# Optimization experiments

Measured on AMD Instinct MI355X. Metric: run time of the kernel, lower is better.

The kernel has to match this reference:

```python
import jax, jax.numpy as jnp
import numpy as np

DIM = 2048
NUM_HEADS = 16
HEAD_DIM = 128
SEQ = 4096
HDIM = NUM_HEADS * HEAD_DIM
EPS = 1e-6


def _rope_tables(seq_len, head_dim):
    quarter = head_dim // 4
    ang = (1.0 / 1024.0) ** np.linspace(0.0, 1.0, quarter, dtype=np.float32)
    ang = np.concatenate([ang, np.zeros(quarter, dtype=np.float32)])  # [head_dim//2]
    theta = np.arange(seq_len, dtype=np.float32)[:, None] * ang[None, :]  # [T, D/2]
    return jnp.asarray(np.cos(theta)), jnp.asarray(np.sin(theta))


def _rms_norm(x):
    return x * jax.lax.rsqrt(jnp.mean(x * x, axis=-1, keepdims=True) + EPS)


def _apply_rope(x, cos, sin):
    # x: [B, T, H, D]; cos/sin: [T, D/2]
    c = cos[None, :, None, :]
    s = sin[None, :, None, :]
    x1, x2 = jnp.split(x, 2, axis=-1)
    return jnp.concatenate([x1 * c + x2 * s, -x1 * s + x2 * c], axis=-1)


def setup_inputs() -> dict:
    key = jax.random.key(0)
    k1, k2, k3, k4, k5 = jax.random.split(key, 5)
    x = jax.random.normal(k1, (1, SEQ, DIM), dtype=jnp.float32)
    ve = jax.random.normal(k2, (1, SEQ, HDIM), dtype=jnp.float32)
    lambdas = jax.random.uniform(k3, (2,), dtype=jnp.float32)
    bound = (3.0 ** 0.5) * 0.5 * DIM ** (-0.5)
    qkv_w = jax.random.uniform(k4, (3, HDIM, DIM), dtype=jnp.float32, minval=-bound, maxval=bound)
    proj_w = 0.02 * jax.random.normal(k5, (DIM, HDIM), dtype=jnp.float32)
    return {"x": x, "ve": ve, "lambdas": lambdas, "qkv_w": qkv_w, "proj_w": proj_w}


def reference(x, ve, lambdas, qkv_w, proj_w):
    B, T, _ = x.shape
    cos, sin = _rope_tables(T, HEAD_DIM)
    # fused QKV projection: qkv_w [3, hdim, dim]
    qkv = jnp.einsum('btd,ced->cbte', x, qkv_w)  # [3, B, T, hdim]
    q, k, v = [a.reshape(B, T, NUM_HEADS, HEAD_DIM) for a in qkv]
    q = _apply_rope(_rms_norm(q), cos, sin)
    k = _apply_rope(_rms_norm(k), cos, sin)
    v = lambdas[0] * v + lambdas[1] * ve.reshape(v.shape)
    # causal SDPA, default scale 1/sqrt(head_dim)
    scale = 1.0 / jnp.sqrt(jnp.float32(HEAD_DIM))
    scores = jnp.einsum('bthd,bshd->bhts', q, k) * scale  # [B, H, T, T]
    causal = jnp.tril(jnp.ones((T, T), dtype=bool))
    scores = jnp.where(causal[None, None], scores, jnp.float32(-1e30))
    probs = jax.nn.softmax(scores, axis=-1)
    out = jnp.einsum('bhts,bshd->bthd', probs, v).reshape(B, T, HDIM)
    return out @ proj_w.T
```

## Files before the change

### kernel.cpp

```cpp
#include <hip/hip_runtime.h>
#include <cstdint>
#include <cstddef>

constexpr int T_SEQ = 4096;
constexpr int NH    = 16;
constexpr int HD    = 128;
constexpr int DIM   = 2048;
constexpr int HDIM  = 2048;

typedef __attribute__((ext_vector_type(8)))  short  short8;
typedef __attribute__((ext_vector_type(4)))  float  f32x4;
typedef __attribute__((ext_vector_type(16))) float  f32x16;
typedef __attribute__((ext_vector_type(8)))  unsigned short u16x8;
typedef __attribute__((ext_vector_type(4)))  unsigned short u16x4;
typedef __attribute__((ext_vector_type(4)))  unsigned uint4v;
typedef __attribute__((ext_vector_type(2)))  int int2v;

__device__ __forceinline__ unsigned short f2bf(float f) {
  unsigned u = __float_as_uint(f);
  return (unsigned short)((u + 0x7FFFu + ((u >> 16) & 1u)) >> 16);
}
__device__ __forceinline__ float bf2f(unsigned short h) {
  return __uint_as_float(((unsigned)h) << 16);
}
__device__ __forceinline__ void gload_lds16(const void* g, void* l) {
  __builtin_amdgcn_global_load_lds((const __attribute__((address_space(1))) void*)g,
                                   (__attribute__((address_space(3))) void*)l, 16, 0, 0);
}
__device__ __forceinline__ int2v plswap(int a, int b) {
  return __builtin_amdgcn_permlane32_swap(a, b, false, false);
}
__device__ __forceinline__ void bar() {
  asm volatile("" ::: "memory");
  __builtin_amdgcn_s_barrier();
  asm volatile("" ::: "memory");
}
#define VMCNT(n) asm volatile("s_waitcnt vmcnt(" #n ")" ::: "memory")

__global__ __launch_bounds__(256) void cvt_f32_bf16(const float* __restrict__ in,
                                                    unsigned short* __restrict__ out, int n4) {
  int i = blockIdx.x * 256 + threadIdx.x;
  if (i < n4) {
    float4 v = ((const float4*)in)[i];
    u16x4 o; o.x = f2bf(v.x); o.y = f2bf(v.y); o.z = f2bf(v.z); o.w = f2bf(v.w);
    ((u16x4*)out)[i] = o;
  }
}

__global__ __launch_bounds__(256) void rope_tables(float* __restrict__ cosT, float* __restrict__ sinT) {
  int idx = blockIdx.x * 256 + threadIdx.x;
  if (idx >= T_SEQ * 64) return;
  int t = idx >> 6, i = idx & 63;
  float ang = (i < 32) ? exp2f(-10.0f * (float)i / 31.0f) : 0.0f;
  float th = (float)t * ang;
  cosT[idx] = cosf(th);
  sinT[idx] = sinf(th);
}

template <int MODE>
__global__ __launch_bounds__(512) void gemm256(const unsigned short* __restrict__ A,
                                               const unsigned short* __restrict__ B,
                                               int K, unsigned short* __restrict__ outb,
                                               float* __restrict__ outf, int N) {
  __shared__ __align__(16) char SM[3 * 49152];
  const int tid = threadIdx.x, w = tid >> 6, lane = tid & 63;
  const int wm = w >> 2, wn = w & 3;
  const int lr = lane >> 4, lc = lane & 15, lc7 = lc & 7;
  const int cpx = gridDim.x >> 3;
  const int idx = (blockIdx.x & 7) * cpx + (blockIdx.x >> 3);
  const int m0 = (idx & 31) * 128, n0 = (idx >> 5) * 256;

  const int arow = lane >> 3;
  const int xcol = ((lane & 7) ^ ((lane >> 3) & 7)) * 8;

  auto stageA = [&](int buf, int t) {
    char* base = SM + buf * 49152;
#pragma unroll
    for (int i = 0; i < 2; i++) {
      int c = w + i * 8;
      gload_lds16(A + (size_t)(m0 + c * 8 + arow) * K + t * 64 + xcol, base + c * 1024);
    }
  };
  auto stageB0 = [&](int buf, int t) {
    char* base = SM + buf * 49152 + 16384;
    gload_lds16(B + (size_t)(n0 + w * 8 + arow) * K + t * 64 + xcol, base + w * 1024);
  };
  auto stageB1 = [&](int buf, int t) {
    char* base = SM + buf * 49152 + 16384;
#pragma unroll
    for (int i = 1; i < 4; i++) {
      int c = w + i * 8;
      gload_lds16(B + (size_t)(n0 + c * 8 + arow) * K + t * 64 + xcol, base + c * 1024);
    }
  };

  f32x4 acc[4][4] = {};
  const int NT = K >> 6;

  stageA(0, 0); stageB0(0, 0); stageB1(0, 0);
  stageA(1, 1); stageB0(1, 1); stageB1(1, 1);
  VMCNT(6);
  bar();

#pragma unroll 1
  for (int t = 0; t < NT; t++) {
    const int c = t % 3, s = (t + 2) % 3;
    const bool st = (t + 2) < NT;
    const char* Ab = SM + c * 49152;
    const char* Bb = Ab + 16384;

    short8 a[4], b[4];
#pragma unroll
    for (int mi = 0; mi < 4; mi++)
      a[mi] = *(const short8*)(Ab + (wm * 64 + mi * 16 + lc) * 128 + ((0 + lr) ^ lc7) * 16);
#pragma unroll
    for (int ni = 0; ni < 4; ni++)
      b[ni] = *(const short8*)(Bb + (wn * 64 + ni * 16 + lc) * 128 + ((0 + lr) ^ lc7) * 16);
    if (st) { stageA(s, t + 2); stageB0(s, t + 2); }
    bar();
    __builtin_amdgcn_s_setprio(1);
#pragma unroll
    for (int mi = 0; mi < 4; mi++)
#pragma unroll
      for (int ni = 0; ni < 4; ni++)
        acc[mi][ni] = __builtin_amdgcn_mfma_f32_16x16x32_bf16(a[mi], b[ni], acc[mi][ni], 0, 0, 0);
    __builtin_amdgcn_s_setprio(0);
    bar();

#pragma unroll
    for (int mi = 0; mi < 4; mi++)
      a[mi] = *(const short8*)(Ab + (wm * 64 + mi * 16 + lc) * 128 + ((4 + lr) ^ lc7) * 16);
#pragma unroll
    for (int ni = 0; ni < 4; ni++)
      b[ni] = *(const short8*)(Bb + (wn * 64 + ni * 16 + lc) * 128 + ((4 + lr) ^ lc7) * 16);
    if (st) stageB1(s, t + 2);
    if (st) { VMCNT(6); } else { VMCNT(0); }
    bar();
    __builtin_amdgcn_s_setprio(1);
#pragma unroll
    for (int mi = 0; mi < 4; mi++)
#pragma unroll
      for (int ni = 0; ni < 4; ni++)
        acc[mi][ni] = __builtin_amdgcn_mfma_f32_16x16x32_bf16(a[mi], b[ni], acc[mi][ni], 0, 0, 0);
    __builtin_amdgcn_s_setprio(0);
    bar();
  }

#pragma unroll
  for (int mi = 0; mi < 4; mi++)
#pragma unroll
    for (int ni = 0; ni < 4; ni++)
#pragma unroll
      for (int r = 0; r < 4; r++) {
        int t = m0 + wm * 64 + mi * 16 + lr * 4 + r;
        int n = n0 + wn * 64 + ni * 16 + lc;
        float v = acc[mi][ni][r];
        if (MODE == 0) {
          int cc = n >> 11, e = n & 2047, h = e >> 7, d = e & 127;
          outb[(((size_t)cc * NH + h) * T_SEQ + t) * HD + d] = f2bf(v);
        } else {
          outf[(size_t)t * N + n] = v;
        }
      }
}

__global__ __launch_bounds__(256) void norm_rope(unsigned short* __restrict__ qkvb,
                                                 const float* __restrict__ cosT,
                                                 const float* __restrict__ sinT) {
  const int tid = threadIdx.x;
  const int li = tid & 15;
  const int row = blockIdx.x * 16 + (tid >> 4);
  const int t = row & (T_SEQ - 1);
  unsigned short* rp = qkvb + (size_t)row * HD + li * 8;
  u16x8 raw = *(const u16x8*)rp;

  float v[8]; float ss = 0.0f;
#pragma unroll
  for (int j = 0; j < 8; j++) { v[j] = bf2f(raw[j]); ss += v[j] * v[j]; }
#pragma unroll
  for (int off = 1; off < 16; off <<= 1) ss += __shfl_xor(ss, off, 16);
  const float rs = rsqrtf(ss * (1.0f / 128.0f) + 1e-6f);

  uint4v rw = __builtin_bit_cast(uint4v, raw);
  uint4v pwv;
  pwv.x = (unsigned)__shfl_xor((int)rw.x, 8, 16);
  pwv.y = (unsigned)__shfl_xor((int)rw.y, 8, 16);
  pwv.z = (unsigned)__shfl_xor((int)rw.z, 8, 16);
  pwv.w = (unsigned)__shfl_xor((int)rw.w, 8, 16);
  u16x8 praw = __builtin_bit_cast(u16x8, pwv);
  float pv[8];
#pragma unroll
  for (int j = 0; j < 8; j++) pv[j] = bf2f(praw[j]);

  const int e0 = (li & 7) * 8;
  const bool hi8 = li >= 8;
  float4 c0 = *(const float4*)(cosT + t * 64 + e0);
  float4 c1 = *(const float4*)(cosT + t * 64 + e0 + 4);
  float4 s0 = *(const float4*)(sinT + t * 64 + e0);
  float4 s1 = *(const float4*)(sinT + t * 64 + e0 + 4);
  float cc[8] = {c0.x, c0.y, c0.z, c0.w, c1.x, c1.y, c1.z, c1.w};
  float sn[8] = {s0.x, s0.y, s0.z, s0.w, s1.x, s1.y, s1.z, s1.w};

  u16x8 o;
#pragma unroll
  for (int j = 0; j < 8; j++) {
    float x1 = hi8 ? pv[j] : v[j];
    float x2 = hi8 ? v[j] : pv[j];
    float r = hi8 ? (-x1 * sn[j] + x2 * cc[j]) : (x1 * cc[j] + x2 * sn[j]);
    o[j] = f2bf(r * rs);
  }
  *(u16x8*)rp = o;
}

__global__ __launch_bounds__(256) void vmix_transpose(const unsigned short* __restrict__ vb,
                                                      const float* __restrict__ ve,
                                                      const float* __restrict__ lam,
                                                      unsigned short* __restrict__ vt) {
  __shared__ float tile[64][65];
  const int h = blockIdx.z, t0 = blockIdx.x * 64, d0 = blockIdx.y * 64;
  const float l0 = lam[0], l1 = lam[1];
  const int tid = threadIdx.x;
  const int tl = tid >> 4, dl4 = (tid & 15) * 4;
#pragma unroll
  for (int i = 0; i < 4; i++) {
    int t_local = tl + i * 16;
    int t = t0 + t_local;
    const unsigned short* vp = vb + ((size_t)h * T_SEQ + t) * HD + d0 + dl4;
    const float* vep = ve + (size_t)t * HDIM + h * HD + d0 + dl4;
    u16x4 vv = *(const u16x4*)vp;
    float4 vef = *(const float4*)vep;
    tile[t_local][dl4 + 0] = l0 * bf2f(vv.x) + l1 * vef.x;
    tile[t_local][dl4 + 1] = l0 * bf2f(vv.y) + l1 * vef.y;
    tile[t_local][dl4 + 2] = l0 * bf2f(vv.z) + l1 * vef.z;
    tile[t_local][dl4 + 3] = l0 * bf2f(vv.w) + l1 * vef.w;
  }
  __syncthreads();
#pragma unroll
  for (int i = 0; i < 2; i++) {
    int idx = tid + i * 256;
    int d_local = idx >> 3, tloc = (idx & 7) * 8;
    u16x8 o;
#pragma unroll
    for (int j = 0; j < 8; j++) o[j] = f2bf(tile[tloc + j][d_local]);
    *(u16x8*)(vt + ((size_t)h * HD + d0 + d_local) * T_SEQ + t0 + tloc) = o;
  }
}

__global__ __launch_bounds__(512)
__attribute__((amdgpu_waves_per_eu(2, 2)))
void attn_fwd(const unsigned short* __restrict__ qb,
              const unsigned short* __restrict__ kb,
              const unsigned short* __restrict__ vt,
              unsigned short* __restrict__ ao) {
  __shared__ __align__(16) char SMEM[131072];
  __shared__ int gctr[2];
  const int bid = blockIdx.x;
  const int h  = (bid & 7) + ((bid >> 7) << 3);
  const int pr = (bid >> 3) & 15;
  const int tid = threadIdx.x, w = tid >> 6, lane = tid & 63;
  const int g = w >> 2, wq = w & 3;
  const int l31 = lane & 31, hi = lane >> 5, r7 = l31 & 7;
  const unsigned short* qh = qb + (size_t)h * T_SEQ * HD;
  const unsigned short* kh = kb + (size_t)h * T_SEQ * HD;
  const unsigned short* vh = vt + (size_t)h * HD * T_SEQ;

  if (tid < 2) gctr[tid] = 0;
  __syncthreads();
  int bcnt = 0;
  auto GBAR = [&]() {
    asm volatile("s_waitcnt lgkmcnt(0)" ::: "memory");
    ++bcnt;
    if (lane == 0)
      __hip_atomic_fetch_add(&gctr[g], 1, __ATOMIC_RELEASE, __HIP_MEMORY_SCOPE_WORKGROUP);
    while (__hip_atomic_load(&gctr[g], __ATOMIC_ACQUIRE, __HIP_MEMORY_SCOPE_WORKGROUP) < 4 * bcnt)
      __builtin_amdgcn_s_sleep(1);
  };

  char* Kbase = SMEM + g * 65536;
  char* Vbase = SMEM + g * 65536 + 32768;

  const int kcrow = lane >> 4, kcol16 = lane & 15;
  const int vcrow = lane >> 3, vslot0 = lane & 7;

  auto STAGE = [&](int buf, int t) {
#pragma unroll
    for (int i = 0; i < 4; i++) {
      int krow = (wq * 4 + i) * 4 + kcrow;
      int kcol = (kcol16 ^ (krow & 7)) * 8;
      gload_lds16(kh + (size_t)(t * 64 + krow) * HD + kcol,
                  Kbase + buf * 16384 + (wq * 4 + i) * 1024);
      int vrow = (wq * 4 + i) * 8 + vcrow;
      int vcol = (vslot0 ^ (vrow & 7)) * 8;
      gload_lds16(vh + (size_t)vrow * T_SEQ + t * 64 + vcol,
                  Vbase + buf * 16384 + (wq * 4 + i) * 1024);
    }
  };

  const float SCL2E = 0.088388347648318447f * 1.44269504f;

#pragma unroll 1
  for (int which = 0; which < 2; ++which) {
    const int qt = which ? pr : (31 - pr);
    const int ng = qt + 1;
    const int q_row = qt * 128 + wq * 32 + l31;

    short8 qf[8];
#pragma unroll
    for (int dk = 0; dk < 8; dk++)
      qf[dk] = *(const short8*)(qh + (size_t)q_row * HD + dk * 16 + hi * 8);

    f32x16 accO[4] = {};
    float m_r = -1e30f, l_r = 0.0f;

    __syncthreads();
    STAGE(0, g);

#pragma unroll 1
    for (int it = 0; it < ng; it++) {
      const int t = 2 * it + g;
      const int cur = it & 1;
      asm volatile("s_waitcnt vmcnt(0)" ::: "memory");
      GBAR();
      if (it + 1 < ng) STAGE(cur ^ 1, t + 2);

      f32x16 accS0 = {}, accS1 = {};
      const char* Kb = Kbase + cur * 16384 + l31 * 256;
      __builtin_amdgcn_s_setprio(1);
#pragma unroll
      for (int dk = 0; dk < 8; dk++) {
        int sl = ((2 * dk + hi) ^ r7) * 16;
        short8 k0 = *(const short8*)(Kb + sl);
        short8 k1 = *(const short8*)(Kb + 32 * 256 + sl);
        accS0 = __builtin_amdgcn_mfma_f32_32x32x16_bf16(k0, qf[dk], accS0, 0, 0, 0);
        accS1 = __builtin_amdgcn_mfma_f32_32x32x16_bf16(k1, qf[dk], accS1, 0, 0, 0);
      }
      __builtin_amdgcn_s_setprio(0);

      float p[32];
      const bool need_mask = (t * 64 + 63) > (qt * 128 + wq * 32);
      if (need_mask) {
#pragma unroll
        for (int r = 0; r < 16; r++) {
          int kv0 = t * 64 + (r & 3) + 8 * (r >> 2) + 4 * hi;
          p[r]      = (kv0      > q_row) ? -1e30f : accS0[r] * SCL2E;
          p[16 + r] = (kv0 + 32 > q_row) ? -1e30f : accS1[r] * SCL2E;
        }
      } else {
#pragma unroll
        for (int r = 0; r < 16; r++) { p[r] = accS0[r] * SCL2E; p[16 + r] = accS1[r] * SCL2E; }
      }

      float t16[16];
#pragma unroll
      for (int i = 0; i < 16; i++) t16[i] = fmaxf(p[i], p[i + 16]);
#pragma unroll
      for (int st = 8; st >= 1; st >>= 1)
#pragma unroll
        for (int i = 0; i < st; i++) t16[i] = fmaxf(t16[i], t16[i + st]);
      int2v mr_ = plswap(__float_as_int(t16[0]), __float_as_int(t16[0]));
      float mx = fmaxf(t16[0], __int_as_float(hi ? mr_.x : mr_.y));

      if (__any(mx > m_r + 8.0f)) {
        float mn = fmaxf(m_r, mx);
        float alpha = exp2f(m_r - mn);
        m_r = mn; l_r *= alpha;
#pragma unroll
        for (int dt = 0; dt < 4; dt++)
#pragma unroll
          for (int r = 0; r < 16; r++) accO[dt][r] *= alpha;
      }

#pragma unroll
      for (int i = 0; i < 32; i++) p[i] = exp2f(p[i] - m_r);
      float s16[16];
#pragma unroll
      for (int i = 0; i < 16; i++) s16[i] = p[i] + p[i + 16];
#pragma unroll
      for (int st = 8; st >= 1; st >>= 1)
#pragma unroll
        for (int i = 0; i < st; i++) s16[i] += s16[i + st];
      int2v sr_ = plswap(__float_as_int(s16[0]), __float_as_int(s16[0]));
      l_r += s16[0] + __int_as_float(hi ? sr_.x : sr_.y);

      unsigned pk[8][2];
#pragma unroll
      for (int o = 0; o < 8; o++)
#pragma unroll
        for (int c = 0; c < 2; c++) {
          float lo = p[(o >> 2) * 16 + (o & 3) * 4 + 2 * c];
          float hi_ = p[(o >> 2) * 16 + (o & 3) * 4 + 2 * c + 1];
          asm("v_cvt_pk_bf16_f32 %0, %1, %2" : "=v"(pk[o][c]) : "v"(lo), "v"(hi_));
        }

      const char* Vb = Vbase + cur * 16384 + l31 * 128;
#pragma unroll
      for (int ks = 0; ks < 4; ks++) {
        int2v s0 = plswap((int)pk[2 * ks][0], (int)pk[2 * ks + 1][0]);
        int2v s1 = plswap((int)pk[2 * ks][1], (int)pk[2 * ks + 1][1]);
        uint4v pw;
        pw.x = (unsigned)s0.x;
        pw.y = (unsigned)s1.x;
        pw.z = (unsigned)s0.y;
        pw.w = (unsigned)s1.y;
        short8 pb = __builtin_bit_cast(short8, pw);
        int sl = ((2 * ks + hi) ^ r7) * 16;
        __builtin_amdgcn_s_setprio(1);
#pragma unroll
        for (int dt = 0; dt < 4; dt++) {
          short8 vf = *(const short8*)(Vb + dt * 32 * 128 + sl);
          accO[dt] = __builtin_amdgcn_mfma_f32_32x32x16_bf16(vf, pb, accO[dt], 0, 0, 0);
        }
        __builtin_amdgcn_s_setprio(0);
      }
    }

    __syncthreads();
    float* SM_acc = (float*)(SMEM + 65536);
    float* SM_ml  = (float*)SMEM;
    const int q_local = wq * 32 + l31;
    if (g == 1) {
#pragma unroll
      for (int dt = 0; dt < 4; dt++)
#pragma unroll
        for (int r = 0; r < 16; r++) {
          int d = 32 * dt + (r & 3) + 8 * (r >> 2) + 4 * hi;
          SM_acc[q_local * 128 + (d ^ l31)] = accO[dt][r];
        }
      if (hi == 0) { SM_ml[q_local * 2] = m_r; SM_ml[q_local * 2 + 1] = l_r; }
    }
    __syncthreads();
    if (g == 0) {
      float mo = SM_ml[q_local * 2], lo = SM_ml[q_local * 2 + 1];
      float m  = fmaxf(m_r, mo);
      float se = exp2f(m_r - m), so = exp2f(mo - m);
      float inv = 1.0f / (l_r * se + lo * so);
#pragma unroll
      for (int dt = 0; dt < 4; dt++)
#pragma unroll
        for (int q4 = 0; q4 < 4; q4++) {
          int dbase = 32 * dt + 8 * q4 + 4 * hi;
          u16x4 o;
#pragma unroll
          for (int j = 0; j < 4; j++) {
            int r = q4 * 4 + j, d = dbase + j;
            float vo = SM_acc[q_local * 128 + (d ^ l31)];
            o[j] = f2bf((accO[dt][r] * se + vo * so) * inv);
          }
          *(u16x4*)(ao + (size_t)q_row * HDIM + h * HD + dbase) = o;
        }
    }
  }
}

extern "C" void kernel_launch(void* const* d_in, const int* in_sizes, int n_in,
                              void* d_out, int out_size, void* d_ws, size_t ws_size,
                              hipStream_t stream) {
  const float* x      = (const float*)d_in[0];
  const float* ve     = (const float*)d_in[1];
  const float* lam    = (const float*)d_in[2];
  const float* qkv_w  = (const float*)d_in[3];
  const float* proj_w = (const float*)d_in[4];
  float* out = (float*)d_out;

  char* p = (char*)d_ws;
  float* cosT = (float*)p;            p += (size_t)T_SEQ * 64 * 4;
  float* sinT = (float*)p;            p += (size_t)T_SEQ * 64 * 4;
  unsigned short* xb   = (unsigned short*)p; p += (size_t)T_SEQ * DIM * 2;
  unsigned short* wqb  = (unsigned short*)p; p += (size_t)3 * HDIM * DIM * 2;
  unsigned short* pwb  = (unsigned short*)p; p += (size_t)DIM * HDIM * 2;
  unsigned short* qkvb = (unsigned short*)p; p += (size_t)3 * NH * T_SEQ * HD * 2;
  unsigned short* vtb  = (unsigned short*)p; p += (size_t)NH * HD * T_SEQ * 2;
  unsigned short* aob  = (unsigned short*)p; p += (size_t)T_SEQ * HDIM * 2;

  cvt_f32_bf16<<<(T_SEQ * DIM / 4 + 255) / 256, 256, 0, stream>>>(x, xb, T_SEQ * DIM / 4);
  cvt_f32_bf16<<<(3 * HDIM * DIM / 4 + 255) / 256, 256, 0, stream>>>(qkv_w, wqb, 3 * HDIM * DIM / 4);
  cvt_f32_bf16<<<(DIM * HDIM / 4 + 255) / 256, 256, 0, stream>>>(proj_w, pwb, DIM * HDIM / 4);
  rope_tables<<<(T_SEQ * 64 + 255) / 256, 256, 0, stream>>>(cosT, sinT);

  gemm256<0><<<768, 512, 0, stream>>>(xb, wqb, DIM, qkvb, nullptr, 3 * HDIM);
  norm_rope<<<2 * NH * T_SEQ / 16, 256, 0, stream>>>(qkvb, cosT, sinT);
  vmix_transpose<<<dim3(T_SEQ / 64, HD / 64, NH), 256, 0, stream>>>(
      qkvb + (size_t)2 * NH * T_SEQ * HD, ve, lam, vtb);
  attn_fwd<<<256, 512, 0, stream>>>(qkvb, qkvb + (size_t)NH * T_SEQ * HD, vtb, aob);
  gemm256<1><<<256, 512, 0, stream>>>(aob, pwb, HDIM, nullptr, out, HDIM);
}
```

Before: 340.7 us.

## Use fixed softmax max bound from RMS-normed Q/K and fold scale into Q

After RMS norm and RoPE, every query and key vector has a fixed norm. That caps the scaled log2 score at about 16.3, so the attention kernel now subtracts a constant 16.5 instead of tracking a running row max. This drops the per-tile max reduction, the cross-lane swap, the conditional rescale of the accumulators, and the max merge between the two key-split halves. The softmax scale and log2e factor move into the q rows of the norm_rope kernel, so the inner loop no longer multiplies by them. The risk is small probabilities underflowing or losing relative precision when actual scores sit far below the bound, and any bf16 rounding that pushes a score slightly past it.

```diff
diff --git a/kernel.cpp b/kernel.cpp
--- a/kernel.cpp
+++ b/kernel.cpp
@@ -179,7 +179,8 @@
   for (int j = 0; j < 8; j++) { v[j] = bf2f(raw[j]); ss += v[j] * v[j]; }
 #pragma unroll
   for (int off = 1; off < 16; off <<= 1) ss += __shfl_xor(ss, off, 16);
-  const float rs = rsqrtf(ss * (1.0f / 128.0f) + 1e-6f);
+  float rs = rsqrtf(ss * (1.0f / 128.0f) + 1e-6f);
+  if (row < NH * T_SEQ) rs *= 0.088388347648318447f * 1.44269504f;
 
   uint4v rw = __builtin_bit_cast(uint4v, raw);
   uint4v pwv;
@@ -296,7 +297,7 @@
     }
   };
 
-  const float SCL2E = 0.088388347648318447f * 1.44269504f;
+  const float FM = 16.5f;
 
 #pragma unroll 1
   for (int which = 0; which < 2; ++which) {
@@ -310,7 +311,7 @@
       qf[dk] = *(const short8*)(qh + (size_t)q_row * HD + dk * 16 + hi * 8);
 
     f32x16 accO[4] = {};
-    float m_r = -1e30f, l_r = 0.0f;
+    float l_r = 0.0f;
 
     __syncthreads();
     STAGE(0, g);
@@ -342,36 +343,17 @@
 #pragma unroll
         for (int r = 0; r < 16; r++) {
           int kv0 = t * 64 + (r & 3) + 8 * (r >> 2) + 4 * hi;
-          p[r]      = (kv0      > q_row) ? -1e30f : accS0[r] * SCL2E;
-          p[16 + r] = (kv0 + 32 > q_row) ? -1e30f : accS1[r] * SCL2E;
+          p[r]      = (kv0      > q_row) ? 0.0f : exp2f(accS0[r] - FM);
+          p[16 + r] = (kv0 + 32 > q_row) ? 0.0f : exp2f(accS1[r] - FM);
         }
       } else {
 #pragma unroll
-        for (int r = 0; r < 16; r++) { p[r] = accS0[r] * SCL2E; p[16 + r] = accS1[r] * SCL2E; }
+        for (int r = 0; r < 16; r++) {
+          p[r]      = exp2f(accS0[r] - FM);
+          p[16 + r] = exp2f(accS1[r] - FM);
+        }
       }
 
-      float t16[16];
-#pragma unroll
-      for (int i = 0; i < 16; i++) t16[i] = fmaxf(p[i], p[i + 16]);
-#pragma unroll
-      for (int st = 8; st >= 1; st >>= 1)
-#pragma unroll
-        for (int i = 0; i < st; i++) t16[i] = fmaxf(t16[i], t16[i + st]);
-      int2v mr_ = plswap(__float_as_int(t16[0]), __float_as_int(t16[0]));
-      float mx = fmaxf(t16[0], __int_as_float(hi ? mr_.x : mr_.y));
-
-      if (__any(mx > m_r + 8.0f)) {
-        float mn = fmaxf(m_r, mx);
-        float alpha = exp2f(m_r - mn);
-        m_r = mn; l_r *= alpha;
-#pragma unroll
-        for (int dt = 0; dt < 4; dt++)
-#pragma unroll
-          for (int r = 0; r < 16; r++) accO[dt][r] *= alpha;
-      }
-
-#pragma unroll
-      for (int i = 0; i < 32; i++) p[i] = exp2f(p[i] - m_r);
       float s16[16];
 #pragma unroll
       for (int i = 0; i < 16; i++) s16[i] = p[i] + p[i + 16];
@@ -416,7 +398,7 @@
 
     __syncthreads();
     float* SM_acc = (float*)(SMEM + 65536);
-    float* SM_ml  = (float*)SMEM;
+    float* SM_l   = (float*)SMEM;
     const int q_local = wq * 32 + l31;
     if (g == 1) {
 #pragma unroll
@@ -426,14 +408,12 @@
           int d = 32 * dt + (r & 3) + 8 * (r >> 2) + 4 * hi;
           SM_acc[q_local * 128 + (d ^ l31)] = accO[dt][r];
         }
-      if (hi == 0) { SM_ml[q_local * 2] = m_r; SM_ml[q_local * 2 + 1] = l_r; }
+      if (hi == 0) SM_l[q_local] = l_r;
     }
     __syncthreads();
     if (g == 0) {
-      float mo = SM_ml[q_local * 2], lo = SM_ml[q_local * 2 + 1];
-      float m  = fmaxf(m_r, mo);
-      float se = exp2f(m_r - m), so = exp2f(mo - m);
-      float inv = 1.0f / (l_r * se + lo * so);
+      float lo = SM_l[q_local];
+      float inv = 1.0f / (l_r + lo);
 #pragma unroll
       for (int dt = 0; dt < 4; dt++)
 #pragma unroll
@@ -444,7 +424,7 @@
           for (int j = 0; j < 4; j++) {
             int r = q4 * 4 + j, d = dbase + j;
             float vo = SM_acc[q_local * 128 + (d ^ l31)];
-            o[j] = f2bf((accO[dt][r] * se + vo * so) * inv);
+            o[j] = f2bf((accO[dt][r] + vo) * inv);
           }
           *(u16x4*)(ao + (size_t)q_row * HDIM + h * HD + dbase) = o;
         }
```

After: 327.9 us. -3.8%, faster.
